# Kernel optimization log

Measured on AMD Instinct MI355X. Metric: run time of the kernel, lower is better.

## Reference

```python
import jax, jax.numpy as jnp
import numpy as np

N = 50000      # nodes
E = 800000     # edges
IN, HID, OUT = 256, 512, 256
EPS = 1e-5     # BatchNorm eps


def setup_inputs() -> dict:
    key = jax.random.key(0)
    ks = jax.random.split(key, 12)
    x = jax.random.normal(ks[0], (N, IN), jnp.float32)
    edge_index = jax.random.randint(ks[1], (2, E), 0, N, jnp.int32)

    def lin(k, fi, fo):
        return jax.random.normal(k, (fi, fo), jnp.float32) / np.sqrt(fi).astype(np.float32)

    return {
        "x": x,
        "edge_index": edge_index,
        "W1": lin(ks[2], IN, HID),  "b1": jnp.zeros((HID,), jnp.float32),
        "g1": jnp.ones((HID,), jnp.float32), "be1": jnp.zeros((HID,), jnp.float32),
        "W2": lin(ks[3], HID, HID), "b2": jnp.zeros((HID,), jnp.float32),
        "g2": jnp.ones((HID,), jnp.float32), "be2": jnp.zeros((HID,), jnp.float32),
        "W3": lin(ks[4], HID, OUT), "b3": jnp.zeros((OUT,), jnp.float32),
    }


def _gcn_conv(x, W, b, src, dst, dinv):
    # PyG GCNConv: D^{-1/2}(A+I)D^{-1/2} X W + b, edge weights = 1
    h = x @ W                                   # [N, F_out] dense transform
    norm = (dinv[src] * dinv[dst])[:, None]     # [E, 1]
    agg = jax.ops.segment_sum(h[src] * norm, dst, num_segments=N)
    agg = agg + h * (dinv * dinv)[:, None]      # self-loop contribution
    return agg + b


def _bn(h, g, b):
    # BatchNorm1d, training-mode batch statistics over node dim
    m = h.mean(axis=0)
    v = h.var(axis=0)
    return (h - m) * jax.lax.rsqrt(v + EPS) * g + b


def reference(x, edge_index, W1, b1, g1, be1, W2, b2, g2, be2, W3, b3):
    src, dst = edge_index[0], edge_index[1]
    # symmetric normalization degrees (incl. self loop)
    deg = jax.ops.segment_sum(jnp.ones((E,), jnp.float32), dst, num_segments=N) + 1.0
    dinv = jax.lax.rsqrt(deg)

    residual = x  # in_feats == out_feats -> nn.Identity
    h = jax.nn.relu(_bn(_gcn_conv(x, W1, b1, src, dst, dinv), g1, be1))
    h = jax.nn.relu(_bn(_gcn_conv(h, W2, b2, src, dst, dinv), g2, be2))
    h = _gcn_conv(h, W3, b3, src, dst, dinv)
    return h + residual
```

## Files before the change

### kernel.cpp

```cpp
#include <hip/hip_runtime.h>
#include <hip/hip_bf16.h>

#define NN 50000
#define NE 800000

typedef unsigned short u16;
typedef unsigned int   u32;

typedef __attribute__((ext_vector_type(8))) __bf16 bf16x8;
typedef __attribute__((ext_vector_type(4))) float  f32x4;

__device__ __forceinline__ float bf2f(u16 x) {
    u32 u = ((u32)x) << 16;
    return __builtin_bit_cast(float, u);
}
__device__ __forceinline__ u16 f2bf(float f) {
    u32 u = __builtin_bit_cast(u32, f);
    u32 r = (u + 0x7FFFu + ((u >> 16) & 1u)) >> 16;
    return (u16)r;
}
__device__ __forceinline__ float bflo(u32 w) { return __builtin_bit_cast(float, w << 16); }
__device__ __forceinline__ float bfhi(u32 w) { return __builtin_bit_cast(float, w & 0xffff0000u); }


__global__ __launch_bounds__(256) void count_k(const int* __restrict__ dst, int* __restrict__ deg, int E) {
    int e = blockIdx.x * 256 + threadIdx.x;
    if (e < E) atomicAdd(&deg[dst[e]], 1);
}

__global__ __launch_bounds__(256) void dinv_k(const int* __restrict__ deg, float* __restrict__ dinv, int n) {
    int i = blockIdx.x * 256 + threadIdx.x;
    if (i < n) dinv[i] = rsqrtf((float)deg[i] + 1.0f);
}

__global__ __launch_bounds__(256) void scan1_k(const int* __restrict__ deg, int* __restrict__ bsum, int n) {
    __shared__ int sd[256];
    int i = blockIdx.x * 256 + threadIdx.x;
    sd[threadIdx.x] = (i < n) ? deg[i] : 0;
    __syncthreads();
    for (int s = 128; s > 0; s >>= 1) {
        if (threadIdx.x < s) sd[threadIdx.x] += sd[threadIdx.x + s];
        __syncthreads();
    }
    if (threadIdx.x == 0) bsum[blockIdx.x] = sd[0];
}

__global__ __launch_bounds__(256) void scan2_k(int* __restrict__ bsum, int nb) {
    __shared__ int sd[256];
    int t = threadIdx.x;
    int v = (t < nb) ? bsum[t] : 0;
    sd[t] = v;
    __syncthreads();
    for (int off = 1; off < 256; off <<= 1) {
        int tv = (t >= off) ? sd[t - off] : 0;
        __syncthreads();
        sd[t] += tv;
        __syncthreads();
    }
    if (t < nb) bsum[t] = sd[t] - v;
}

__global__ __launch_bounds__(256) void scan3_k(const int* __restrict__ deg, const int* __restrict__ bofs,
                                               int* __restrict__ rs, int* __restrict__ cur, int n) {
    __shared__ int sd[256];
    int t = threadIdx.x;
    int i = blockIdx.x * 256 + t;
    int v = (i < n) ? deg[i] : 0;
    sd[t] = v;
    __syncthreads();
    for (int off = 1; off < 256; off <<= 1) {
        int tv = (t >= off) ? sd[t - off] : 0;
        __syncthreads();
        sd[t] += tv;
        __syncthreads();
    }
    int excl = sd[t] - v + bofs[blockIdx.x];
    if (i < n) { rs[i] = excl; cur[i] = excl; }
}

__global__ __launch_bounds__(256) void fill_k(const int* __restrict__ src, const int* __restrict__ dst,
                                              int* __restrict__ cur, int* __restrict__ csr, int E) {
    int e = blockIdx.x * 256 + threadIdx.x;
    if (e < E) {
        int d = dst[e];
        int pos = atomicAdd(&cur[d], 1);
        csr[pos] = src[e];
    }
}


__global__ __launch_bounds__(256) void cast_k(const float* __restrict__ X, u16* __restrict__ Y, int total) {
    int idx = (blockIdx.x * 256 + threadIdx.x) * 8;
    if (idx >= total) return;
    float4 a = *(const float4*)(X + idx);
    float4 b = *(const float4*)(X + idx + 4);
    uint4 o;
    o.x = (u32)f2bf(a.x) | ((u32)f2bf(a.y) << 16);
    o.y = (u32)f2bf(a.z) | ((u32)f2bf(a.w) << 16);
    o.z = (u32)f2bf(b.x) | ((u32)f2bf(b.y) << 16);
    o.w = (u32)f2bf(b.z) | ((u32)f2bf(b.w) << 16);
    *(uint4*)(Y + idx) = o;
}


__global__ __launch_bounds__(256) void transpose_k(const float* __restrict__ W, u16* __restrict__ Wt, int K, int F) {
    __shared__ float t[32][33];
    int k0 = blockIdx.x * 32, f0 = blockIdx.y * 32;
    int tx = threadIdx.x & 31, ty = threadIdx.x >> 5;
    for (int r = ty; r < 32; r += 8) t[r][tx] = W[(size_t)(k0 + r) * F + f0 + tx];
    __syncthreads();
    for (int r = ty; r < 32; r += 8) Wt[(size_t)(f0 + r) * K + k0 + tx] = f2bf(t[tx][r]);
}


template <int F, int MODE>
__global__ __launch_bounds__(256) void aggu_k(const u16* __restrict__ X, u16* __restrict__ Y,
                                              float* __restrict__ Yf,
                                              const float* __restrict__ dinv, const int* __restrict__ rs,
                                              const int* __restrict__ dg, const int* __restrict__ csr,
                                              const float* __restrict__ scale, const float* __restrict__ shift,
                                              const float* __restrict__ b3, const float* __restrict__ xres) {
    constexpr int FB = F / 64;
    const int tid = threadIdx.x;
    const int lane = tid & 63;
    const int i = blockIdx.x * 4 + (tid >> 6);
    if (i >= NN) return;
    const int start = rs[i], cnt = dg[i];
    const float di = dinv[i];

    float sc[FB], sh[FB];
    if constexpr (MODE == 1) {
        #pragma unroll
        for (int k = 0; k < FB; k++) {
            sc[k] = scale[lane * FB + k];
            sh[k] = shift[lane * FB + k];
        }
    }

    float acc[FB];
    #pragma unroll
    for (int k = 0; k < FB; k++) acc[k] = 0.f;

    auto gadd = [&](int row, float wgt) {
        float v[FB];
        if constexpr (FB == 4) {
            uint2 p = *(const uint2*)(X + (size_t)row * F + lane * 4);
            v[0] = bflo(p.x); v[1] = bfhi(p.x);
            v[2] = bflo(p.y); v[3] = bfhi(p.y);
        } else {
            uint4 p = *(const uint4*)(X + (size_t)row * F + lane * 8);
            v[0] = bflo(p.x); v[1] = bfhi(p.x);
            v[2] = bflo(p.y); v[3] = bfhi(p.y);
            v[4] = bflo(p.z); v[5] = bfhi(p.z);
            v[6] = bflo(p.w); v[7] = bfhi(p.w);
        }
        #pragma unroll
        for (int k = 0; k < FB; k++) {
            if constexpr (MODE == 1) v[k] = fmaxf(fmaf(v[k], sc[k], sh[k]), 0.f);
            acc[k] = fmaf(v[k], wgt, acc[k]);
        }
    };

    gadd(i, di);

    for (int base = 0; base < cnt; base += 64) {
        const int m = min(64, cnt - base);
        int   sidx = 0;
        float sw   = 0.f;
        if (lane < m) {
            sidx = csr[start + base + lane];
            sw   = dinv[sidx];
        }
        int j = 0;
        for (; j + 4 <= m; j += 4) {
            int   r0 = __shfl(sidx, j + 0), r1 = __shfl(sidx, j + 1);
            int   r2 = __shfl(sidx, j + 2), r3 = __shfl(sidx, j + 3);
            float w0 = __shfl(sw, j + 0), w1 = __shfl(sw, j + 1);
            float w2 = __shfl(sw, j + 2), w3 = __shfl(sw, j + 3);
            gadd(r0, w0);
            gadd(r1, w1);
            gadd(r2, w2);
            gadd(r3, w3);
        }
        for (; j < m; j++) gadd(__shfl(sidx, j), __shfl(sw, j));
    }

    if constexpr (MODE == 2) {
        float4 xr = *(const float4*)(xres + (size_t)i * 256 + lane * 4);
        float4 bb = *(const float4*)(b3 + lane * 4);
        float4 o;
        o.x = acc[0] * di + bb.x + xr.x;
        o.y = acc[1] * di + bb.y + xr.y;
        o.z = acc[2] * di + bb.z + xr.z;
        o.w = acc[3] * di + bb.w + xr.w;
        *(float4*)(Yf + (size_t)i * 256 + lane * 4) = o;
    } else if constexpr (FB == 4) {
        uint2 o;
        o.x = (u32)f2bf(acc[0] * di) | ((u32)f2bf(acc[1] * di) << 16);
        o.y = (u32)f2bf(acc[2] * di) | ((u32)f2bf(acc[3] * di) << 16);
        *(uint2*)(Y + (size_t)i * F + lane * 4) = o;
    } else {
        uint4 o;
        o.x = (u32)f2bf(acc[0] * di) | ((u32)f2bf(acc[1] * di) << 16);
        o.y = (u32)f2bf(acc[2] * di) | ((u32)f2bf(acc[3] * di) << 16);
        o.z = (u32)f2bf(acc[4] * di) | ((u32)f2bf(acc[5] * di) << 16);
        o.w = (u32)f2bf(acc[6] * di) | ((u32)f2bf(acc[7] * di) << 16);
        *(uint4*)(Y + (size_t)i * F + lane * 8) = o;
    }
}


template <int MODE>
__global__ __launch_bounds__(256) void aggp_k(const u16* __restrict__ X, u16* __restrict__ Y,
                                              float* __restrict__ Yf,
                                              const float* __restrict__ dinv, const int* __restrict__ rs,
                                              const int* __restrict__ dg, const int* __restrict__ csr,
                                              const float* __restrict__ b3, const float* __restrict__ xres) {
    const int tid  = threadIdx.x;
    const int lane = tid & 63;
    const int hf   = lane >> 5;
    const int fl   = lane & 31;
    const int i = blockIdx.x * 4 + (tid >> 6);
    if (i >= NN) return;
    const int start = rs[i], cnt = dg[i];
    const float di = dinv[i];

    float acc[8];
    #pragma unroll
    for (int k = 0; k < 8; k++) acc[k] = 0.f;

    auto gadd = [&](int row, float wgt) {
        uint4 q = *(const uint4*)(X + (size_t)row * 256 + fl * 8);
        float v[8];
        v[0] = bflo(q.x); v[1] = bfhi(q.x);
        v[2] = bflo(q.y); v[3] = bfhi(q.y);
        v[4] = bflo(q.z); v[5] = bfhi(q.z);
        v[6] = bflo(q.w); v[7] = bfhi(q.w);
        #pragma unroll
        for (int k = 0; k < 8; k++) acc[k] = fmaf(v[k], wgt, acc[k]);
    };

    gadd(i, hf ? 0.f : di);

    for (int base = 0; base < cnt; base += 64) {
        const int m = min(64, cnt - base);
        int   sidx = 0;
        float sw   = 0.f;
        if (lane < m) {
            sidx = csr[start + base + lane];
            sw   = dinv[sidx];
        }
        int j = 0;
        for (; j + 8 <= m; j += 8) {
            int   r0 = __shfl(sidx, j + 0 + hf), r1 = __shfl(sidx, j + 2 + hf);
            int   r2 = __shfl(sidx, j + 4 + hf), r3 = __shfl(sidx, j + 6 + hf);
            float w0 = __shfl(sw, j + 0 + hf), w1 = __shfl(sw, j + 2 + hf);
            float w2 = __shfl(sw, j + 4 + hf), w3 = __shfl(sw, j + 6 + hf);
            gadd(r0, w0);
            gadd(r1, w1);
            gadd(r2, w2);
            gadd(r3, w3);
        }
        for (; j < m; j += 2) {
            gadd(__shfl(sidx, j + hf), __shfl(sw, j + hf));
        }
    }

    #pragma unroll
    for (int k = 0; k < 8; k++) acc[k] += __shfl_xor(acc[k], 32);

    if (hf == 0) {
        if constexpr (MODE == 2) {
            const float* xr = xres + (size_t)i * 256 + fl * 8;
            float4 x0 = *(const float4*)xr;
            float4 x1 = *(const float4*)(xr + 4);
            float4 b0 = *(const float4*)(b3 + fl * 8);
            float4 b1 = *(const float4*)(b3 + fl * 8 + 4);
            float4 o0, o1;
            o0.x = acc[0] * di + b0.x + x0.x; o0.y = acc[1] * di + b0.y + x0.y;
            o0.z = acc[2] * di + b0.z + x0.z; o0.w = acc[3] * di + b0.w + x0.w;
            o1.x = acc[4] * di + b1.x + x1.x; o1.y = acc[5] * di + b1.y + x1.y;
            o1.z = acc[6] * di + b1.z + x1.z; o1.w = acc[7] * di + b1.w + x1.w;
            float* yp = Yf + (size_t)i * 256 + fl * 8;
            *(float4*)yp = o0;
            *(float4*)(yp + 4) = o1;
        } else {
            uint4 o;
            o.x = (u32)f2bf(acc[0] * di) | ((u32)f2bf(acc[1] * di) << 16);
            o.y = (u32)f2bf(acc[2] * di) | ((u32)f2bf(acc[3] * di) << 16);
            o.z = (u32)f2bf(acc[4] * di) | ((u32)f2bf(acc[5] * di) << 16);
            o.w = (u32)f2bf(acc[6] * di) | ((u32)f2bf(acc[7] * di) << 16);
            *(uint4*)(Y + (size_t)i * 256 + fl * 8) = o;
        }
    }
}


template <bool STATS, bool BIAS>
__global__ __launch_bounds__(256) void gemm_k(const u16* __restrict__ A, const u16* __restrict__ Wt,
                                              const float* __restrict__ bias, u16* __restrict__ C,
                                              float* __restrict__ colsum, float* __restrict__ colsq,
                                              int M, int K, int F) {
    __shared__ u16 As[128 * 40];
    __shared__ u16 Bs[128 * 40];
    const int m0 = blockIdx.x * 128, f0 = blockIdx.y * 128;
    const int tid = threadIdx.x;
    const int lane = tid & 63, wave = tid >> 6;
    const int waveM = (wave >> 1) * 64, waveN = (wave & 1) * 64;
    const int lrow = tid >> 2, lch = tid & 3;

    f32x4 acc[4][4];
    const f32x4 fz = {0.f, 0.f, 0.f, 0.f};
    #pragma unroll
    for (int i = 0; i < 4; i++)
        #pragma unroll
        for (int j = 0; j < 4; j++) acc[i][j] = fz;

    const int rA0 = m0 + lrow, rA1 = m0 + 64 + lrow;
    const u16* pA0 = A + (size_t)rA0 * K + lch * 8;
    const u16* pA1 = A + (size_t)rA1 * K + lch * 8;
    const u16* pB0 = Wt + (size_t)(f0 + lrow) * K + lch * 8;
    const u16* pB1 = Wt + (size_t)(f0 + 64 + lrow) * K + lch * 8;
    u16* qA0 = &As[lrow * 40 + lch * 8];
    u16* qA1 = &As[(64 + lrow) * 40 + lch * 8];
    u16* qB0 = &Bs[lrow * 40 + lch * 8];
    u16* qB1 = &Bs[(64 + lrow) * 40 + lch * 8];
    const uint4 z4 = {0u, 0u, 0u, 0u};

    const int fm = lane & 15, fq = lane >> 4;

    for (int k0 = 0; k0 < K; k0 += 32) {
        uint4 a0 = (rA0 < M) ? *(const uint4*)(pA0 + k0) : z4;
        uint4 a1 = (rA1 < M) ? *(const uint4*)(pA1 + k0) : z4;
        uint4 b0 = *(const uint4*)(pB0 + k0);
        uint4 b1 = *(const uint4*)(pB1 + k0);
        __syncthreads();
        *(uint4*)qA0 = a0;
        *(uint4*)qA1 = a1;
        *(uint4*)qB0 = b0;
        *(uint4*)qB1 = b1;
        __syncthreads();
        bf16x8 af[4], bfr[4];
        #pragma unroll
        for (int i = 0; i < 4; i++)
            af[i] = *(const bf16x8*)&As[(waveM + i * 16 + fm) * 40 + fq * 8];
        #pragma unroll
        for (int j = 0; j < 4; j++)
            bfr[j] = *(const bf16x8*)&Bs[(waveN + j * 16 + fm) * 40 + fq * 8];
        #pragma unroll
        for (int i = 0; i < 4; i++)
            #pragma unroll
            for (int j = 0; j < 4; j++)
                acc[i][j] = __builtin_amdgcn_mfma_f32_16x16x32_bf16(af[i], bfr[j], acc[i][j], 0, 0, 0);
    }

    #pragma unroll
    for (int j = 0; j < 4; j++) {
        const int col = f0 + waveN + j * 16 + fm;
        const float bcol = BIAS ? bias[col] : 0.f;
        float s = 0.f, s2 = 0.f;
        #pragma unroll
        for (int i = 0; i < 4; i++) {
            const int rb = m0 + waveM + i * 16 + fq * 4;
            #pragma unroll
            for (int r = 0; r < 4; r++) {
                const int row = rb + r;
                if (row < M) {
                    float v = acc[i][j][r] + bcol;
                    C[(size_t)row * F + col] = f2bf(v);
                    if (STATS) { s += v; s2 += v * v; }
                }
            }
        }
        if (STATS) {
            s += __shfl_xor(s, 16);
            s += __shfl_xor(s, 32);
            s2 += __shfl_xor(s2, 16);
            s2 += __shfl_xor(s2, 32);
            if (fq == 0) {
                atomicAdd(&colsum[col], s);
                atomicAdd(&colsq[col], s2);
            }
        }
    }
}


__global__ __launch_bounds__(256) void bnfin_k(const float* __restrict__ sum, const float* __restrict__ sq,
                                               const float* __restrict__ g, const float* __restrict__ be,
                                               float* __restrict__ scale, float* __restrict__ shift,
                                               int F, float invN) {
    int f = blockIdx.x * 256 + threadIdx.x;
    if (f < F) {
        float m = sum[f] * invN;
        float v = sq[f] * invN - m * m;
        float s = rsqrtf(v + 1e-5f) * g[f];
        scale[f] = s;
        shift[f] = be[f] - m * s;
    }
}

__global__ __launch_bounds__(256) void bnrelu_k(u16* __restrict__ H, const float* __restrict__ scale,
                                                const float* __restrict__ shift, int total, int F) {
    int idx = blockIdx.x * 256 + threadIdx.x;
    int base = idx * 8;
    if (base >= total) return;
    uint4 p = *(const uint4*)(H + base);
    int col = base & (F - 1);
    u32 w[4] = {p.x, p.y, p.z, p.w};
    u32 o[4];
    #pragma unroll
    for (int q = 0; q < 4; q++) {
        float x0 = fmaxf(bflo(w[q]) * scale[col + 2 * q] + shift[col + 2 * q], 0.f);
        float x1 = fmaxf(bfhi(w[q]) * scale[col + 2 * q + 1] + shift[col + 2 * q + 1], 0.f);
        o[q] = ((u32)f2bf(x1) << 16) | (u32)f2bf(x0);
    }
    uint4 po = {o[0], o[1], o[2], o[3]};
    *(uint4*)(H + base) = po;
}


extern "C" void kernel_launch(void* const* d_in, const int* in_sizes, int n_in,
                              void* d_out, int out_size, void* d_ws, size_t ws_size,
                              hipStream_t stream) {
    const float* x   = (const float*)d_in[0];
    const int*   ei  = (const int*)d_in[1];
    const float* W1  = (const float*)d_in[2];
    const float* b1  = (const float*)d_in[3];
    const float* pg1 = (const float*)d_in[4];
    const float* pbe1= (const float*)d_in[5];
    const float* W2  = (const float*)d_in[6];
    const float* b2  = (const float*)d_in[7];
    const float* pg2 = (const float*)d_in[8];
    const float* pbe2= (const float*)d_in[9];
    const float* W3  = (const float*)d_in[10];
    const float* b3  = (const float*)d_in[11];
    float* out = (float*)d_out;

    char* ws = (char*)d_ws;
    size_t off = 0;
    auto alloc = [&](size_t bytes) -> char* {
        char* p = ws + off;
        off += (bytes + 255) & ~(size_t)255;
        return p;
    };
    float* dinv  = (float*)alloc(NN * 4);
    int*   deg   = (int*)alloc(NN * 4);
    int*   rs    = (int*)alloc(NN * 4);
    int*   cur   = (int*)alloc(NN * 4);
    int*   bsum  = (int*)alloc(256 * 4);
    int*   csr   = (int*)alloc(NE * 4);
    float* stats = (float*)alloc(4 * 512 * 4);
    float* cs1 = stats, *cq1 = stats + 512, *cs2 = stats + 1024, *cq2 = stats + 1536;
    float* scale1 = (float*)alloc(512 * 4);
    float* shift1 = (float*)alloc(512 * 4);
    float* scale2 = (float*)alloc(512 * 4);
    float* shift2 = (float*)alloc(512 * 4);
    u16*   W1t   = (u16*)alloc((size_t)512 * 256 * 2);
    u16*   W2t   = (u16*)alloc((size_t)512 * 512 * 2);
    u16*   W3t   = (u16*)alloc((size_t)256 * 512 * 2);
    u16*   HB    = (u16*)alloc((size_t)NN * 512 * 2);
    u16*   G3    = (u16*)alloc((size_t)NN * 256 * 2);

    u16* XB = G3;
    u16* A1 = (u16*)d_out;
    u16* A2 = (u16*)d_out;

    const int* srcp = ei;
    const int* dstp = ei + NE;

    hipMemsetAsync(deg, 0, NN * 4, stream);
    hipMemsetAsync(stats, 0, 4 * 512 * 4, stream);

    const int nbN = (NN + 255) / 256;
    count_k<<<(NE + 255) / 256, 256, 0, stream>>>(dstp, deg, NE);
    dinv_k<<<nbN, 256, 0, stream>>>(deg, dinv, NN);
    scan1_k<<<nbN, 256, 0, stream>>>(deg, bsum, NN);
    scan2_k<<<1, 256, 0, stream>>>(bsum, nbN);
    scan3_k<<<nbN, 256, 0, stream>>>(deg, bsum, rs, cur, NN);
    fill_k<<<(NE + 255) / 256, 256, 0, stream>>>(srcp, dstp, cur, csr, NE);

    transpose_k<<<dim3(256 / 32, 512 / 32), 256, 0, stream>>>(W1, W1t, 256, 512);
    transpose_k<<<dim3(512 / 32, 512 / 32), 256, 0, stream>>>(W2, W2t, 512, 512);
    transpose_k<<<dim3(512 / 32, 256 / 32), 256, 0, stream>>>(W3, W3t, 512, 256);

    cast_k<<<NN * 256 / 8 / 256, 256, 0, stream>>>(x, XB, NN * 256);

    const int MT = (NN + 127) / 128;
    const int AGB = (NN + 3) / 4;

    aggp_k<0><<<AGB, 256, 0, stream>>>(XB, A1, nullptr, dinv, rs, deg, csr,
                                       nullptr, nullptr);
    gemm_k<true, true><<<dim3(MT, 4), 256, 0, stream>>>(A1, W1t, b1, HB, cs1, cq1, NN, 256, 512);
    bnfin_k<<<2, 256, 0, stream>>>(cs1, cq1, pg1, pbe1, scale1, shift1, 512, 1.f / NN);

    aggu_k<512, 1><<<AGB, 256, 0, stream>>>(HB, A2, nullptr, dinv, rs, deg, csr,
                                            scale1, shift1, nullptr, nullptr);
    gemm_k<true, true><<<dim3(MT, 4), 256, 0, stream>>>(A2, W2t, b2, HB, cs2, cq2, NN, 512, 512);
    bnfin_k<<<2, 256, 0, stream>>>(cs2, cq2, pg2, pbe2, scale2, shift2, 512, 1.f / NN);
    bnrelu_k<<<NN * 512 / 8 / 256, 256, 0, stream>>>(HB, scale2, shift2, NN * 512, 512);

    gemm_k<false, false><<<dim3(MT, 2), 256, 0, stream>>>(HB, W3t, nullptr, G3, nullptr, nullptr, NN, 512, 256);
    aggp_k<2><<<AGB, 256, 0, stream>>>(G3, nullptr, out, dinv, rs, deg, csr,
                                       b3, x);
}
```

Measured before the change: 693.5 us.

## Use direct global-to-LDS loads in GEMM and readlane broadcasts in aggregation

The GEMM staging now uses global_load_lds to copy A and B tiles straight into shared memory without passing through registers. It also drops the padded 40-element row stride for a dense 32 stride and clamps out-of-range rows instead of zero-filling. The aggregation kernel makes the node index wave-uniform and replaces shuffles with readlane scalar broadcasts, unrolling 8 neighbors per step for more outstanding loads. Risks are LDS bank conflicts from the unpadded layout, possible missing waits before the barrier for the async LDS loads, and clamped rows feeding duplicate data into the bias/statistics epilogue if it is not masked.

```diff
diff --git a/kernel.cpp b/kernel.cpp
--- a/kernel.cpp
+++ b/kernel.cpp
@@ -21,6 +21,18 @@
 }
 __device__ __forceinline__ float bflo(u32 w) { return __builtin_bit_cast(float, w << 16); }
 __device__ __forceinline__ float bfhi(u32 w) { return __builtin_bit_cast(float, w & 0xffff0000u); }
+
+__device__ __forceinline__ int rl_i(int v, int j) {
+    return __builtin_amdgcn_readlane(v, j);
+}
+__device__ __forceinline__ float rl_f(float v, int j) {
+    return __builtin_bit_cast(float, __builtin_amdgcn_readlane(__builtin_bit_cast(int, v), j));
+}
+
+__device__ __forceinline__ void glds16(const u16* g, u16* l) {
+    __builtin_amdgcn_global_load_lds((const __attribute__((address_space(1))) void*)g,
+                                     (__attribute__((address_space(3))) void*)l, 16, 0, 0);
+}
 
 
 __global__ __launch_bounds__(256) void count_k(const int* __restrict__ dst, int* __restrict__ deg, int E) {
@@ -123,7 +135,7 @@
     constexpr int FB = F / 64;
     const int tid = threadIdx.x;
     const int lane = tid & 63;
-    const int i = blockIdx.x * 4 + (tid >> 6);
+    const int i = __builtin_amdgcn_readfirstlane(blockIdx.x * 4 + (tid >> 6));
     if (i >= NN) return;
     const int start = rs[i], cnt = dg[i];
     const float di = dinv[i];
@@ -142,17 +154,18 @@
     for (int k = 0; k < FB; k++) acc[k] = 0.f;
 
     auto gadd = [&](int row, float wgt) {
+        const u16* p = X + (size_t)row * F + lane * FB;
         float v[FB];
         if constexpr (FB == 4) {
-            uint2 p = *(const uint2*)(X + (size_t)row * F + lane * 4);
-            v[0] = bflo(p.x); v[1] = bfhi(p.x);
-            v[2] = bflo(p.y); v[3] = bfhi(p.y);
+            uint2 q = *(const uint2*)p;
+            v[0] = bflo(q.x); v[1] = bfhi(q.x);
+            v[2] = bflo(q.y); v[3] = bfhi(q.y);
         } else {
-            uint4 p = *(const uint4*)(X + (size_t)row * F + lane * 8);
-            v[0] = bflo(p.x); v[1] = bfhi(p.x);
-            v[2] = bflo(p.y); v[3] = bfhi(p.y);
-            v[4] = bflo(p.z); v[5] = bfhi(p.z);
-            v[6] = bflo(p.w); v[7] = bfhi(p.w);
+            uint4 q = *(const uint4*)p;
+            v[0] = bflo(q.x); v[1] = bfhi(q.x);
+            v[2] = bflo(q.y); v[3] = bfhi(q.y);
+            v[4] = bflo(q.z); v[5] = bfhi(q.z);
+            v[6] = bflo(q.w); v[7] = bfhi(q.w);
         }
         #pragma unroll
         for (int k = 0; k < FB; k++) {
@@ -172,17 +185,18 @@
             sw   = dinv[sidx];
         }
         int j = 0;
-        for (; j + 4 <= m; j += 4) {
-            int   r0 = __shfl(sidx, j + 0), r1 = __shfl(sidx, j + 1);
-            int   r2 = __shfl(sidx, j + 2), r3 = __shfl(sidx, j + 3);
-            float w0 = __shfl(sw, j + 0), w1 = __shfl(sw, j + 1);
-            float w2 = __shfl(sw, j + 2), w3 = __shfl(sw, j + 3);
-            gadd(r0, w0);
-            gadd(r1, w1);
-            gadd(r2, w2);
-            gadd(r3, w3);
-        }
-        for (; j < m; j++) gadd(__shfl(sidx, j), __shfl(sw, j));
+        for (; j + 8 <= m; j += 8) {
+            int   r[8];
+            float w[8];
+            #pragma unroll
+            for (int q = 0; q < 8; q++) {
+                r[q] = rl_i(sidx, j + q);
+                w[q] = rl_f(sw, j + q);
+            }
+            #pragma unroll
+            for (int q = 0; q < 8; q++) gadd(r[q], w[q]);
+        }
+        for (; j < m; j++) gadd(rl_i(sidx, j), rl_f(sw, j));
     }
 
     if constexpr (MODE == 2) {
@@ -301,8 +315,8 @@
                                               const float* __restrict__ bias, u16* __restrict__ C,
                                               float* __restrict__ colsum, float* __restrict__ colsq,
                                               int M, int K, int F) {
-    __shared__ u16 As[128 * 40];
-    __shared__ u16 Bs[128 * 40];
+    __shared__ u16 As[128 * 32];
+    __shared__ u16 Bs[128 * 32];
     const int m0 = blockIdx.x * 128, f0 = blockIdx.y * 128;
     const int tid = threadIdx.x;
     const int lane = tid & 63, wave = tid >> 6;
@@ -317,36 +331,33 @@
         for (int j = 0; j < 4; j++) acc[i][j] = fz;
 
     const int rA0 = m0 + lrow, rA1 = m0 + 64 + lrow;
-    const u16* pA0 = A + (size_t)rA0 * K + lch * 8;
-    const u16* pA1 = A + (size_t)rA1 * K + lch * 8;
+    const int cA0 = (rA0 < M) ? rA0 : (M - 1);
+    const int cA1 = (rA1 < M) ? rA1 : (M - 1);
+    const u16* pA0 = A + (size_t)cA0 * K + lch * 8;
+    const u16* pA1 = A + (size_t)cA1 * K + lch * 8;
     const u16* pB0 = Wt + (size_t)(f0 + lrow) * K + lch * 8;
     const u16* pB1 = Wt + (size_t)(f0 + 64 + lrow) * K + lch * 8;
-    u16* qA0 = &As[lrow * 40 + lch * 8];
-    u16* qA1 = &As[(64 + lrow) * 40 + lch * 8];
-    u16* qB0 = &Bs[lrow * 40 + lch * 8];
-    u16* qB1 = &Bs[(64 + lrow) * 40 + lch * 8];
-    const uint4 z4 = {0u, 0u, 0u, 0u};
+    u16* qA0 = &As[tid * 8];
+    u16* qA1 = &As[2048 + tid * 8];
+    u16* qB0 = &Bs[tid * 8];
+    u16* qB1 = &Bs[2048 + tid * 8];
 
     const int fm = lane & 15, fq = lane >> 4;
 
     for (int k0 = 0; k0 < K; k0 += 32) {
-        uint4 a0 = (rA0 < M) ? *(const uint4*)(pA0 + k0) : z4;
-        uint4 a1 = (rA1 < M) ? *(const uint4*)(pA1 + k0) : z4;
-        uint4 b0 = *(const uint4*)(pB0 + k0);
-        uint4 b1 = *(const uint4*)(pB1 + k0);
-        __syncthreads();
-        *(uint4*)qA0 = a0;
-        *(uint4*)qA1 = a1;
-        *(uint4*)qB0 = b0;
-        *(uint4*)qB1 = b1;
+        __syncthreads();
+        glds16(pA0 + k0, qA0);
+        glds16(pA1 + k0, qA1);
+        glds16(pB0 + k0, qB0);
+        glds16(pB1 + k0, qB1);
         __syncthreads();
         bf16x8 af[4], bfr[4];
         #pragma unroll
         for (int i = 0; i < 4; i++)
-            af[i] = *(const bf16x8*)&As[(waveM + i * 16 + fm) * 40 + fq * 8];
+            af[i] = *(const bf16x8*)&As[(waveM + i * 16 + fm) * 32 + fq * 8];
         #pragma unroll
         for (int j = 0; j < 4; j++)
-            bfr[j] = *(const bf16x8*)&Bs[(waveN + j * 16 + fm) * 40 + fq * 8];
+            bfr[j] = *(const bf16x8*)&Bs[(waveN + j * 16 + fm) * 32 + fq * 8];
         #pragma unroll
         for (int i = 0; i < 4; i++)
             #pragma unroll
```

Measured after the change: 693.1 us. No clear change (-0.1%).
